# Kernel optimization log

Hardware: AMD Instinct MI355X
Metric: run time of the kernel (lower is better)

The kernel has to match this reference:

```python
import jax, jax.numpy as jnp
import numpy as np

CODE_SIZE = 8
NUM_HEADS = 16
KC = 2 ** CODE_SIZE  # 256 codebook buckets


def setup_inputs() -> dict:
    key = jax.random.key(0)
    ks = jax.random.split(key, 6)
    B, Lq, Lk, C = 8, 2048, 4096, 1024
    q = jax.random.normal(ks[0], (B * Lq, C), jnp.float32)
    k = jax.random.normal(ks[1], (B * Lk, C), jnp.float32)
    v = jax.random.normal(ks[2], (B * Lk, C), jnp.float32)
    Wc = jax.random.normal(ks[3], (CODE_SIZE, C), jnp.float32) * (C ** -0.5)  # code_proj weight
    bc = jnp.zeros((CODE_SIZE,), jnp.float32)                                  # code_proj bias
    codebook = jax.random.normal(ks[4], (2 * CODE_SIZE, C), jnp.float32) * 0.02
    lengths = jnp.full((B,), Lk, jnp.int32)      # kv tokens per sample
    inv_lengths = jnp.full((B,), Lq, jnp.int32)  # q tokens per sample
    return dict(q=q, k=k, v=v, Wc=Wc, bc=bc, codebook=codebook,
                lengths=lengths, inv_lengths=inv_lengths)


def reference(q, k, v, Wc, bc, codebook, lengths, inv_lengths):
    C = q.shape[-1]
    d = C // NUM_HEADS
    scale = d ** -0.5
    B = lengths.shape[0]
    Lk = k.shape[0] // B  # equal per-sample kv lengths
    Lq = q.shape[0] // B  # equal per-sample q lengths

    # --- binary spherical quantization of k ---
    code = k @ Wc.T + bc
    code = code / jnp.linalg.norm(code, axis=-1, keepdims=True)
    # sign in {-1,+1}/sqrt(cs); affine *sqrt(cs)/2 + 0.5 -> bits in {0,1}
    bits = (code >= 0).astype(jnp.int32)                      # [B*Lk, cs]
    code_base = 2 ** jnp.arange(CODE_SIZE - 1, -1, -1)        # [cs]
    idxs = (bits * code_base).sum(-1)                         # [B*Lk] in [0, 256)

    # --- dense codebook keys for all 2^cs codes ---
    base_bits = (jnp.arange(KC)[:, None] // code_base) % 2    # [K, cs]
    base = jnp.concatenate([base_bits, 1 - base_bits], axis=-1).astype(codebook.dtype)  # [K, 2cs]
    cod_k = base @ codebook                                   # [K, C]

    # --- scatter-add v and counts into per-sample buckets ---
    b_idx = jnp.repeat(jnp.arange(B), Lk)                     # batch id per kv token
    flat = b_idx * KC + idxs                                  # [B*Lk]
    cod_v = jax.ops.segment_sum(v, flat, num_segments=B * KC).reshape(B, KC, C)
    counts = jax.ops.segment_sum(jnp.ones((B * Lk,), q.dtype), flat,
                                 num_segments=B * KC).reshape(B, KC)

    # --- bucketed attention with quotient normalization ---
    qh = q.reshape(B, Lq, NUM_HEADS, d)
    kh = cod_k.reshape(KC, NUM_HEADS, d)
    vh = cod_v.reshape(B, KC, NUM_HEADS, d)
    scores = scale * jnp.einsum('blhd,khd->blhk', qh, kh)     # [B,Lq,H,K]
    bias = jnp.where(counts > 0, 0.0, -jnp.inf)[:, None, None, :]  # mask empty buckets
    attn = jax.nn.softmax(scores + bias, axis=-1)
    num = jnp.einsum('blhk,bkhd->blhd', attn, vh)             # attn @ summed-v
    den = jnp.einsum('blhk,bk->blh', attn, counts)            # attn @ counts
    out = num / den[..., None]
    return out.reshape(B * Lq, C)
```

## Files before the change

### kernel.cpp

```cpp
#include <hip/hip_runtime.h>
#include <hip/hip_bf16.h>

constexpr int B  = 8;
constexpr int LQ = 2048;
constexpr int LK = 4096;
constexpr int C  = 1024;
constexpr int H  = 16;
constexpr int D  = 64;
constexpr int CS = 8;
constexpr int KC = 256;
constexpr float SCALE = 0.125f;

typedef __attribute__((ext_vector_type(8))) short short8;
typedef __attribute__((ext_vector_type(4))) float f32x4;

union FragU { unsigned u[4]; short8 s; float4 f; };

__device__ inline unsigned bfp(float a, float b) {
  float2 f2; f2.x = a; f2.y = b;
  __hip_bfloat162 h = __float22bfloat162_rn(f2);
  return *reinterpret_cast<unsigned*>(&h);
}
__device__ inline unsigned short bf1(float a) {
  __hip_bfloat16 h = __float2bfloat16(a);
  return *reinterpret_cast<unsigned short*>(&h);
}

__global__ __launch_bounds__(256) void k_codes(
    const float* __restrict__ kmat, const float* __restrict__ Wc,
    const float* __restrict__ bc, int* __restrict__ idx,
    float* __restrict__ counts)
{
  __shared__ float wS[CS * C];
  const int tid = threadIdx.x;
  {
    const float4* wsrc = (const float4*)Wc;
    float4* wdst = (float4*)wS;
#pragma unroll
    for (int i = 0; i < 8; ++i) wdst[tid + i * 256] = wsrc[tid + i * 256];
  }
  __syncthreads();

  const int wave = tid >> 6, lane = tid & 63;

  for (int i = 0; i < 8; ++i) {
    const int r = blockIdx.x * 32 + wave * 8 + i;
    const float4* krow = (const float4*)(kmat + (size_t)r * C);
    float acc[CS];
#pragma unroll
    for (int j = 0; j < CS; ++j) acc[j] = 0.f;
#pragma unroll
    for (int rep = 0; rep < 4; ++rep) {
      float4 kv = krow[rep * 64 + lane];
      const int dbase = (rep * 64 + lane) * 4;
#pragma unroll
      for (int j = 0; j < CS; ++j) {
        float4 wv = *(const float4*)&wS[j * C + dbase];
        acc[j] += kv.x * wv.x + kv.y * wv.y + kv.z * wv.z + kv.w * wv.w;
      }
    }
#pragma unroll
    for (int j = 0; j < CS; ++j) {
#pragma unroll
      for (int off = 32; off >= 1; off >>= 1)
        acc[j] += __shfl_xor(acc[j], off, 64);
    }
    if (lane == 0) {
      int ix = 0;
#pragma unroll
      for (int j = 0; j < CS; ++j) {
        float cj = acc[j] + bc[j];
        ix |= (cj >= 0.f ? 1 : 0) << (7 - j);
      }
      idx[r] = ix;
      const int bb = r >> 12;
      atomicAdd(&counts[bb * KC + ix], 1.0f);
    }
  }
}

__global__ __launch_bounds__(256) void k_offsets(
    const float* __restrict__ counts, int* __restrict__ offs,
    int* __restrict__ cursor, float4* __restrict__ vfc)
{
  __shared__ int wsum[4];
  const int b = blockIdx.x, t = threadIdx.x;
  const int lane = t & 63, w = t >> 6;
  const int myc = (int)counts[b * KC + t];
  int scan = myc;
#pragma unroll
  for (int off = 1; off < 64; off <<= 1) {
    int u = __shfl_up(scan, off, 64);
    if (lane >= off) scan += u;
  }
  if (lane == 63) wsum[w] = scan;
  __syncthreads();
  int base = 0;
#pragma unroll
  for (int i = 0; i < 4; ++i) base += (i < w) ? wsum[i] : 0;
  const int excl = base + scan - myc;
  offs[b * KC + t]   = b * LK + excl;
  cursor[b * KC + t] = b * LK + excl;

  for (int i = t; i < 512; i += 256) {
    const int qc = i >> 6, ln = i & 63;
    FragU u4;
    if ((ln & 15) == 0) {
      const int o = qc * 4 + (ln >> 4);
      const float* cs = counts + b * KC + o * 8;
      u4.u[0] = bfp(cs[0], cs[1]); u4.u[1] = bfp(cs[2], cs[3]);
      u4.u[2] = bfp(cs[4], cs[5]); u4.u[3] = bfp(cs[6], cs[7]);
    } else {
      u4.u[0] = u4.u[1] = u4.u[2] = u4.u[3] = 0u;
    }
    vfc[b * 512 + i] = u4.f;
  }
}

__global__ __launch_bounds__(256) void k_permute(
    const int* __restrict__ idx, int* __restrict__ cursor,
    int* __restrict__ perm)
{
  const int r = blockIdx.x * 256 + threadIdx.x;
  const int b = r >> 12;
  const int ix = idx[r];
  const int pos = atomicAdd(&cursor[b * KC + ix], 1);
  perm[pos] = r;
}

__global__ __launch_bounds__(256) void k_gather(
    const float* __restrict__ v, const int* __restrict__ perm,
    const int* __restrict__ offs, const float* __restrict__ counts,
    unsigned short* __restrict__ vbf)
{
  __shared__ int permS[512];
  const int t = threadIdx.x;
  const int ix = blockIdx.x, b = blockIdx.y;
  const int start = offs[b * KC + ix];
  const int cnt = (int)counts[b * KC + ix];

  float4 acc = make_float4(0.f, 0.f, 0.f, 0.f);
  for (int base = 0; base < cnt; base += 512) {
    const int n = min(512, cnt - base);
    __syncthreads();
    for (int i = t; i < n; i += 256) permS[i] = perm[start + base + i];
    __syncthreads();
    int i = 0;
    for (; i + 4 <= n; i += 4) {
      const int r0 = permS[i], r1 = permS[i + 1];
      const int r2 = permS[i + 2], r3 = permS[i + 3];
      float4 a = *(const float4*)(v + (size_t)r0 * C + t * 4);
      float4 b4 = *(const float4*)(v + (size_t)r1 * C + t * 4);
      float4 c4 = *(const float4*)(v + (size_t)r2 * C + t * 4);
      float4 d4 = *(const float4*)(v + (size_t)r3 * C + t * 4);
      acc.x += a.x + b4.x + c4.x + d4.x;
      acc.y += a.y + b4.y + c4.y + d4.y;
      acc.z += a.z + b4.z + c4.z + d4.z;
      acc.w += a.w + b4.w + c4.w + d4.w;
    }
    for (; i < n; ++i) {
      const int r0 = permS[i];
      float4 a = *(const float4*)(v + (size_t)r0 * C + t * 4);
      acc.x += a.x; acc.y += a.y; acc.z += a.z; acc.w += a.w;
    }
  }

  const int h = t >> 4;
  const int n0 = (t & 15) * 4;
  const int o = ix >> 3, r = ix & 7;
  const int slot0 = ((o >> 2) * 4 + (n0 >> 4)) * 64 + (o & 3) * 16 + (n0 & 15);
  unsigned short* dst = vbf + ((size_t)((b * 16 + h) * 2048 + slot0)) * 8 + r;
  dst[0]  = bf1(acc.x);
  dst[8]  = bf1(acc.y);
  dst[16] = bf1(acc.z);
  dst[24] = bf1(acc.w);
}

__global__ __launch_bounds__(256) void k_attn(
    const float* __restrict__ q, const float* __restrict__ cb,
    const float4* __restrict__ vfb, const float4* __restrict__ vfc,
    float* __restrict__ out)
{
  __shared__ __align__(16) char smem[18432];
  float4* QA  = (float4*)smem;
  float4* CBf = (float4*)(smem + 16384);
  float*  TS  = (float*)smem;

  const int tid = threadIdx.x;
  const int lane = tid & 63, wq = tid >> 6, quad = lane >> 4;
  const int h = blockIdx.y, b = blockIdx.z;
  const int q0 = blockIdx.x * 128;

#pragma unroll
  for (int it = 0; it < 4; ++it) {
    const int od = tid & 7, m = it * 32 + (tid >> 3);
    const float* src = q + (size_t)(b * LQ + q0 + m) * C + h * D + od * 8;
    float4 f0 = *(const float4*)src, f1 = *(const float4*)(src + 4);
    FragU u;
    u.u[0] = bfp(f0.x * SCALE, f0.y * SCALE);
    u.u[1] = bfp(f0.z * SCALE, f0.w * SCALE);
    u.u[2] = bfp(f1.x * SCALE, f1.y * SCALE);
    u.u[3] = bfp(f1.z * SCALE, f1.w * SCALE);
    QA[((m >> 4) * 2 + (od >> 2)) * 64 + (od & 3) * 16 + (m & 15)] = u.f;
  }
  if (tid < 128) {
    const int od = tid & 7, j = tid >> 3;
    const float* src = cb + (size_t)j * C + h * D + od * 8;
    float4 f0 = *(const float4*)src, f1 = *(const float4*)(src + 4);
    FragU u;
    u.u[0] = bfp(f0.x, f0.y); u.u[1] = bfp(f0.z, f0.w);
    u.u[2] = bfp(f1.x, f1.y); u.u[3] = bfp(f1.z, f1.w);
    CBf[(od >> 2) * 64 + (od & 3) * 16 + j] = u.f;
  }
  __syncthreads();

  f32x4 tacc[2];
#pragma unroll
  for (int mt2 = 0; mt2 < 2; ++mt2) {
    const int mt = wq * 2 + mt2;
    FragU a0, a1, b0, b1;
    a0.f = QA[(mt * 2 + 0) * 64 + lane];
    a1.f = QA[(mt * 2 + 1) * 64 + lane];
    b0.f = CBf[0 * 64 + lane];
    b1.f = CBf[1 * 64 + lane];
    f32x4 z = {0.f, 0.f, 0.f, 0.f};
    z = __builtin_amdgcn_mfma_f32_16x16x32_bf16(a0.s, b0.s, z, 0, 0, 0);
    z = __builtin_amdgcn_mfma_f32_16x16x32_bf16(a1.s, b1.s, z, 0, 0, 0);
    tacc[mt2] = z;
  }
  __syncthreads();

#pragma unroll
  for (int mt2 = 0; mt2 < 2; ++mt2) {
    const int mt = wq * 2 + mt2;
#pragma unroll
    for (int r = 0; r < 4; ++r)
      TS[mt * 272 + (quad * 4 + r) * 17 + (lane & 15)] = tacc[mt2][r];
  }
  float t0[16], t1[16];
#pragma unroll
  for (int j = 0; j < 16; ++j) {
    t0[j] = TS[(wq * 2 + 0) * 272 + (lane & 15) * 17 + j];
    t1[j] = TS[(wq * 2 + 1) * 272 + (lane & 15) * 17 + j];
  }

  float esl0[8], esl1[8];
#pragma unroll
  for (int c = 0; c < 8; ++c) {
    esl0[c] = __expf(((c & 4) ? t0[5] : t0[13]) + ((c & 2) ? t0[6] : t0[14]) +
                     ((c & 1) ? t0[7] : t0[15]));
    esl1[c] = __expf(((c & 4) ? t1[5] : t1[13]) + ((c & 2) ? t1[6] : t1[14]) +
                     ((c & 1) ? t1[7] : t1[15]));
  }

  f32x4 acc[2][5];
#pragma unroll
  for (int i = 0; i < 2; ++i)
#pragma unroll
    for (int t_ = 0; t_ < 5; ++t_) acc[i][t_] = (f32x4){0.f, 0.f, 0.f, 0.f};

  const float4* vb = vfb + (size_t)(b * 16 + h) * 2048 + lane;
  const float4* vc = vfc + b * 512 + lane;

#pragma unroll
  for (int qc = 0; qc < 8; ++qc) {
    FragU bf0, bf1_, bf2, bf3, cf;
    bf0.f = vb[(qc * 4 + 0) * 64];
    bf1_.f = vb[(qc * 4 + 1) * 64];
    bf2.f = vb[(qc * 4 + 2) * 64];
    bf3.f = vb[(qc * 4 + 3) * 64];
    cf.f  = vc[qc * 64];

    const int u = qc * 4 + quad;
    const float eshi0 = __expf(
        ((u & 16) ? t0[0] : t0[8]) + ((u & 8) ? t0[1] : t0[9]) +
        ((u & 4) ? t0[2] : t0[10]) + ((u & 2) ? t0[3] : t0[11]) +
        ((u & 1) ? t0[4] : t0[12]));
    const float eshi1 = __expf(
        ((u & 16) ? t1[0] : t1[8]) + ((u & 8) ? t1[1] : t1[9]) +
        ((u & 4) ? t1[2] : t1[10]) + ((u & 2) ? t1[3] : t1[11]) +
        ((u & 1) ? t1[4] : t1[12]));

    FragU a0, a1;
    a0.u[0] = bfp(eshi0 * esl0[0], eshi0 * esl0[1]);
    a0.u[1] = bfp(eshi0 * esl0[2], eshi0 * esl0[3]);
    a0.u[2] = bfp(eshi0 * esl0[4], eshi0 * esl0[5]);
    a0.u[3] = bfp(eshi0 * esl0[6], eshi0 * esl0[7]);
    a1.u[0] = bfp(eshi1 * esl1[0], eshi1 * esl1[1]);
    a1.u[1] = bfp(eshi1 * esl1[2], eshi1 * esl1[3]);
    a1.u[2] = bfp(eshi1 * esl1[4], eshi1 * esl1[5]);
    a1.u[3] = bfp(eshi1 * esl1[6], eshi1 * esl1[7]);

    acc[0][0] = __builtin_amdgcn_mfma_f32_16x16x32_bf16(a0.s, bf0.s,  acc[0][0], 0, 0, 0);
    acc[1][0] = __builtin_amdgcn_mfma_f32_16x16x32_bf16(a1.s, bf0.s,  acc[1][0], 0, 0, 0);
    acc[0][1] = __builtin_amdgcn_mfma_f32_16x16x32_bf16(a0.s, bf1_.s, acc[0][1], 0, 0, 0);
    acc[1][1] = __builtin_amdgcn_mfma_f32_16x16x32_bf16(a1.s, bf1_.s, acc[1][1], 0, 0, 0);
    acc[0][2] = __builtin_amdgcn_mfma_f32_16x16x32_bf16(a0.s, bf2.s,  acc[0][2], 0, 0, 0);
    acc[1][2] = __builtin_amdgcn_mfma_f32_16x16x32_bf16(a1.s, bf2.s,  acc[1][2], 0, 0, 0);
    acc[0][3] = __builtin_amdgcn_mfma_f32_16x16x32_bf16(a0.s, bf3.s,  acc[0][3], 0, 0, 0);
    acc[1][3] = __builtin_amdgcn_mfma_f32_16x16x32_bf16(a1.s, bf3.s,  acc[1][3], 0, 0, 0);
    acc[0][4] = __builtin_amdgcn_mfma_f32_16x16x32_bf16(a0.s, cf.s,   acc[0][4], 0, 0, 0);
    acc[1][4] = __builtin_amdgcn_mfma_f32_16x16x32_bf16(a1.s, cf.s,   acc[1][4], 0, 0, 0);
  }

  const int srcl = lane & 48;
#pragma unroll
  for (int mt2 = 0; mt2 < 2; ++mt2) {
#pragma unroll
    for (int r = 0; r < 4; ++r) {
      const float den = __shfl(acc[mt2][4][r], srcl, 64);
      const float inv = 1.0f / den;
      const int row = q0 + wq * 32 + mt2 * 16 + quad * 4 + r;
      float* op = out + (size_t)(b * LQ + row) * C + h * D + (lane & 15);
#pragma unroll
      for (int t_ = 0; t_ < 4; ++t_) op[t_ * 16] = acc[mt2][t_][r] * inv;
    }
  }
}

extern "C" void kernel_launch(void* const* d_in, const int* in_sizes, int n_in,
                              void* d_out, int out_size, void* d_ws, size_t ws_size,
                              hipStream_t stream) {
  (void)in_sizes; (void)n_in; (void)out_size; (void)ws_size;
  const float* q  = (const float*)d_in[0];
  const float* k  = (const float*)d_in[1];
  const float* v  = (const float*)d_in[2];
  const float* Wc = (const float*)d_in[3];
  const float* bc = (const float*)d_in[4];
  const float* cb = (const float*)d_in[5];
  float* out = (float*)d_out;

  char* ws = (char*)d_ws;
  int*    idxp = (int*)ws;
  float*  cntp = (float*)(ws + 0x20000);
  int*    offsp = (int*)(ws + 0x22000);
  int*    cursp = (int*)(ws + 0x24000);
  int*    permp = (int*)(ws + 0x26000);
  float4* vfcp  = (float4*)(ws + 0x46000);
  unsigned short* vbfp = (unsigned short*)(ws + 0x60000);

  hipMemsetAsync(cntp, 0, B * KC * sizeof(float), stream);
  hipLaunchKernelGGL(k_codes, dim3(1024), dim3(256), 0, stream,
                     k, Wc, bc, idxp, cntp);
  hipLaunchKernelGGL(k_offsets, dim3(B), dim3(256), 0, stream,
                     cntp, offsp, cursp, vfcp);
  hipLaunchKernelGGL(k_permute, dim3(B * LK / 256), dim3(256), 0, stream,
                     idxp, cursp, permp);
  hipLaunchKernelGGL(k_gather, dim3(KC, B), dim3(256), 0, stream,
                     v, permp, offsp, cntp, vbfp);
  hipLaunchKernelGGL(k_attn, dim3(LQ / 128, H, B), dim3(256), 0, stream,
                     q, cb, (const float4*)vbfp, (const float4*)vfcp, out);
}
```

Before: 378.6 us.

## Fuse histogram, scan and permutation into a single per-batch counting-sort kernel

Global atomic counting in k_codes, the memset, k_offsets and k_permute are replaced by one k_sort kernel, one block per batch. Each block loads its 4096 codes into shared memory, builds a histogram with shared atomics, scans it, and scatters the permutation using shared-memory cursors. This removes a memset and a kernel launch and moves global atomics into LDS. The trade-off is that only 8 blocks do the sort serially, and counts are now stored as ints.

```diff
diff --git a/kernel.cpp b/kernel.cpp
--- a/kernel.cpp
+++ b/kernel.cpp
@@ -28,8 +28,7 @@
 
 __global__ __launch_bounds__(256) void k_codes(
     const float* __restrict__ kmat, const float* __restrict__ Wc,
-    const float* __restrict__ bc, int* __restrict__ idx,
-    float* __restrict__ counts)
+    const float* __restrict__ bc, int* __restrict__ idx)
 {
   __shared__ float wS[CS * C];
   const int tid = threadIdx.x;
@@ -39,6 +38,9 @@
 #pragma unroll
     for (int i = 0; i < 8; ++i) wdst[tid + i * 256] = wsrc[tid + i * 256];
   }
+  float bcr[CS];
+#pragma unroll
+  for (int j = 0; j < CS; ++j) bcr[j] = bc[j];
   __syncthreads();
 
   const int wave = tid >> 6, lane = tid & 63;
@@ -68,25 +70,35 @@
     if (lane == 0) {
       int ix = 0;
 #pragma unroll
-      for (int j = 0; j < CS; ++j) {
-        float cj = acc[j] + bc[j];
-        ix |= (cj >= 0.f ? 1 : 0) << (7 - j);
-      }
+      for (int j = 0; j < CS; ++j)
+        ix |= ((acc[j] + bcr[j]) >= 0.f ? 1 : 0) << (7 - j);
       idx[r] = ix;
-      const int bb = r >> 12;
-      atomicAdd(&counts[bb * KC + ix], 1.0f);
-    }
-  }
-}
-
-__global__ __launch_bounds__(256) void k_offsets(
-    const float* __restrict__ counts, int* __restrict__ offs,
-    int* __restrict__ cursor, float4* __restrict__ vfc)
+    }
+  }
+}
+
+__global__ __launch_bounds__(256) void k_sort(
+    const int* __restrict__ idx, int* __restrict__ offs,
+    int* __restrict__ cnti, int* __restrict__ perm,
+    float4* __restrict__ vfc)
 {
+  __shared__ int idxS[LK];
+  __shared__ int hist[KC];
+  __shared__ int cur[KC];
   __shared__ int wsum[4];
   const int b = blockIdx.x, t = threadIdx.x;
   const int lane = t & 63, w = t >> 6;
-  const int myc = (int)counts[b * KC + t];
+
+  hist[t] = 0;
+  __syncthreads();
+  for (int i = t; i < LK; i += 256) {
+    const int ix = idx[b * LK + i];
+    idxS[i] = ix;
+    atomicAdd(&hist[ix], 1);
+  }
+  __syncthreads();
+
+  const int myc = hist[t];
   int scan = myc;
 #pragma unroll
   for (int off = 1; off < 64; off <<= 1) {
@@ -98,18 +110,26 @@
   int base = 0;
 #pragma unroll
   for (int i = 0; i < 4; ++i) base += (i < w) ? wsum[i] : 0;
-  const int excl = base + scan - myc;
-  offs[b * KC + t]   = b * LK + excl;
-  cursor[b * KC + t] = b * LK + excl;
+  const int start = b * LK + base + scan - myc;
+  offs[b * KC + t] = start;
+  cnti[b * KC + t] = myc;
+  cur[t] = start;
+  __syncthreads();
+
+  for (int i = t; i < LK; i += 256) {
+    const int pos = atomicAdd(&cur[idxS[i]], 1);
+    perm[pos] = b * LK + i;
+  }
 
   for (int i = t; i < 512; i += 256) {
     const int qc = i >> 6, ln = i & 63;
     FragU u4;
     if ((ln & 15) == 0) {
-      const int o = qc * 4 + (ln >> 4);
-      const float* cs = counts + b * KC + o * 8;
-      u4.u[0] = bfp(cs[0], cs[1]); u4.u[1] = bfp(cs[2], cs[3]);
-      u4.u[2] = bfp(cs[4], cs[5]); u4.u[3] = bfp(cs[6], cs[7]);
+      const int* cs = hist + (qc * 4 + (ln >> 4)) * 8;
+      u4.u[0] = bfp((float)cs[0], (float)cs[1]);
+      u4.u[1] = bfp((float)cs[2], (float)cs[3]);
+      u4.u[2] = bfp((float)cs[4], (float)cs[5]);
+      u4.u[3] = bfp((float)cs[6], (float)cs[7]);
     } else {
       u4.u[0] = u4.u[1] = u4.u[2] = u4.u[3] = 0u;
     }
@@ -117,27 +137,16 @@
   }
 }
 
-__global__ __launch_bounds__(256) void k_permute(
-    const int* __restrict__ idx, int* __restrict__ cursor,
-    int* __restrict__ perm)
-{
-  const int r = blockIdx.x * 256 + threadIdx.x;
-  const int b = r >> 12;
-  const int ix = idx[r];
-  const int pos = atomicAdd(&cursor[b * KC + ix], 1);
-  perm[pos] = r;
-}
-
 __global__ __launch_bounds__(256) void k_gather(
     const float* __restrict__ v, const int* __restrict__ perm,
-    const int* __restrict__ offs, const float* __restrict__ counts,
+    const int* __restrict__ offs, const int* __restrict__ cnti,
     unsigned short* __restrict__ vbf)
 {
   __shared__ int permS[512];
   const int t = threadIdx.x;
   const int ix = blockIdx.x, b = blockIdx.y;
   const int start = offs[b * KC + ix];
-  const int cnt = (int)counts[b * KC + ix];
+  const int cnt = cnti[b * KC + ix];
 
   float4 acc = make_float4(0.f, 0.f, 0.f, 0.f);
   for (int base = 0; base < cnt; base += 512) {
@@ -331,23 +340,19 @@
   float* out = (float*)d_out;
 
   char* ws = (char*)d_ws;
-  int*    idxp = (int*)ws;
-  float*  cntp = (float*)(ws + 0x20000);
-  int*    offsp = (int*)(ws + 0x22000);
-  int*    cursp = (int*)(ws + 0x24000);
-  int*    permp = (int*)(ws + 0x26000);
-  float4* vfcp  = (float4*)(ws + 0x46000);
+  int*    idxp  = (int*)ws;
+  int*    offsp = (int*)(ws + 0x20000);
+  int*    cntip = (int*)(ws + 0x22000);
+  int*    permp = (int*)(ws + 0x24000);
+  float4* vfcp  = (float4*)(ws + 0x44000);
   unsigned short* vbfp = (unsigned short*)(ws + 0x60000);
 
-  hipMemsetAsync(cntp, 0, B * KC * sizeof(float), stream);
   hipLaunchKernelGGL(k_codes, dim3(1024), dim3(256), 0, stream,
-                     k, Wc, bc, idxp, cntp);
-  hipLaunchKernelGGL(k_offsets, dim3(B), dim3(256), 0, stream,
-                     cntp, offsp, cursp, vfcp);
-  hipLaunchKernelGGL(k_permute, dim3(B * LK / 256), dim3(256), 0, stream,
-                     idxp, cursp, permp);
+                     k, Wc, bc, idxp);
+  hipLaunchKernelGGL(k_sort, dim3(B), dim3(256), 0, stream,
+                     idxp, offsp, cntip, permp, vfcp);
   hipLaunchKernelGGL(k_gather, dim3(KC, B), dim3(256), 0, stream,
-                     v, permp, offsp, cntp, vbfp);
+                     v, permp, offsp, cntip, vbfp);
   hipLaunchKernelGGL(k_attn, dim3(LQ / 128, H, B), dim3(256), 0, stream,
                      q, cb, (const float4*)vbfp, (const float4*)vfcp, out);
 }
```

Result: no change. 375.2 us (-0.9%).
